# Optimization experiments

Hardware: AMD Instinct MI355X
Metric: run time of the kernel (lower is better)

The kernel has to match this reference:

```python
import jax, jax.numpy as jnp
import numpy as np

B, N, D, P = 32, 16, 64, 8  # batch, num_objs, in_feat_dim, patch size
PAIRS = N * (N - 1)


def _conv_relu(x, W, b):
    # Conv2d(kernel=3, stride=1, padding=1) + ReLU, NCHW/OIHW layout
    y = jax.lax.conv_general_dilated(
        x, W, window_strides=(1, 1), padding='SAME',
        dimension_numbers=('NCHW', 'OIHW', 'NCHW'))
    return jax.nn.relu(y + b[None, :, None, None])


def setup_inputs() -> dict:
    key = jax.random.key(0)
    ks = jax.random.split(key, 12)
    x = jax.random.normal(ks[0], (B, N, D, P, P), jnp.float32)
    # g_idx: cols 0,1 index into the repeated pair axis of size N*(N-1); col 2 is a 0/1 mask
    i0 = jax.random.randint(ks[1], (B, PAIRS, 1), 0, PAIRS)
    i1 = jax.random.randint(ks[2], (B, PAIRS, 1), 0, PAIRS)
    m = jax.random.randint(ks[3], (B, PAIRS, 1), 0, 2)
    g_idx = jnp.concatenate([i0, i1, m], axis=2)

    def w(k, o, i):
        return jax.random.normal(k, (o, i, 3, 3), jnp.float32) * (1.0 / np.sqrt(i * 9.0))

    return {
        'x': x, 'g_idx': g_idx,
        'W_rel': w(ks[4], D, 2 * D), 'b_rel': jnp.zeros((D,), jnp.float32),
        'W_self': w(ks[5], D, D), 'b_self': jnp.zeros((D,), jnp.float32),
        'W_aff': w(ks[6], D, D), 'b_aff': jnp.zeros((D,), jnp.float32),
        'W_agg': w(ks[7], D, 2 * D), 'b_agg': jnp.zeros((D,), jnp.float32),
    }


def reference(x, g_idx, W_rel, b_rel, W_self, b_self, W_aff, b_aff, W_agg, b_agg):
    b, n, d, p, _ = x.shape
    pairs = n * (n - 1)
    s = x
    # x1: [B, N*(N-1), D, P, P]
    x1 = jnp.tile(x, (1, n - 1, 1, 1, 1))

    def gather_pair(col):
        idx = g_idx[:, :, col][:, :, None, None, None]  # [B, pairs, 1, 1, 1]
        idx = jnp.broadcast_to(idx, (b, pairs, d, p, p))
        return jnp.take_along_axis(x1, idx, axis=1)

    y1 = gather_pair(0)
    y2 = gather_pair(1)
    mask = g_idx[:, :, 2][:, :, None, None, None].astype(x.dtype)
    r = jnp.concatenate([y1, y2], axis=2) * mask  # [B, pairs, 2D, P, P]
    r = _conv_relu(r.reshape(-1, 2 * d, p, p), W_rel, b_rel)
    r = r.reshape(b, n, n - 1, d, p, p).sum(axis=2)  # scatter-sum per object

    xs = _conv_relu(x.reshape(-1, d, p, p), W_self, b_self).reshape(b, n, d, p, p)
    pred = xs + r
    a = _conv_relu(pred.reshape(-1, d, p, p), W_aff, b_aff).reshape(b, n, d, p, p)
    a = jnp.concatenate([a, s], axis=2)  # [B, N, 2D, P, P]
    out = _conv_relu(a.reshape(-1, 2 * d, p, p), W_agg, b_agg).reshape(b, n, d, p, p)
    return out
```

## Files before the change

### kernel.cpp

```cpp
#include <hip/hip_runtime.h>


#define NIMG 512
#define IMGSZ 4096

using bf16x8 = __attribute__((ext_vector_type(8))) short;
using f32x4  = __attribute__((ext_vector_type(4))) float;
using u16x8  = __attribute__((ext_vector_type(8))) unsigned short;

__device__ inline unsigned short f2bf(float f) {
  union { float f; unsigned u; } v; v.f = f;
  unsigned r = v.u + 0x7fffu + ((v.u >> 16) & 1u);
  return (unsigned short)(r >> 16);
}

__device__ inline f32x4 bf4_to_f32(uint2 p) {
  union { unsigned u; float f; } c;
  f32x4 r;
  c.u = (p.x & 0xffffu) << 16;  r[0] = c.f;
  c.u = (p.x & 0xffff0000u);    r[1] = c.f;
  c.u = (p.y & 0xffffu) << 16;  r[2] = c.f;
  c.u = (p.y & 0xffff0000u);    r[3] = c.f;
  return r;
}

__global__ __launch_bounds__(256) void prep_w(
    const float* __restrict__ Wr, const float* __restrict__ Ws,
    const float* __restrict__ Wa, const float* __restrict__ Wg,
    unsigned short* __restrict__ Wt)
{
  int idx = blockIdx.x * 256 + threadIdx.x;
  if (idx >= 221184) return;
  float v;
  if (idx < 73728) {
    int c = idx / 36864, r = idx % 36864;
    int t = r >> 12, oc = (r >> 6) & 63, ic = r & 63;
    v = (c == 0 ? Ws : Wa)[oc * 576 + ic * 9 + t];
  } else {
    int r2 = idx - 73728;
    int half = r2 / 73728, rr = r2 % 73728;
    int t = rr >> 13, oc = (rr >> 7) & 63, ic = rr & 127;
    v = (half ? Wg : Wr)[oc * 1152 + ic * 9 + t];
  }
  Wt[idx] = f2bf(v);
}

__device__ inline void decode_img(int j, int& b, int& o) {
  b = ((j >> 7) << 3) | (j & 7);
  o = (j >> 3) & 15;
}

template<int ROWX>
__device__ inline void stage_x(const float* __restrict__ xb,
                               unsigned short* __restrict__ s,
                               int coff, int w, int px) {
#pragma unroll
  for (int r = 0; r < 8; ++r) {
    int ic0 = (w + 4 * r) * 2;
    const float* sp = xb + ic0 * 64;
    float a = sp[px], c = sp[64 + px];
    *(unsigned*)(s + px * ROWX + coff + ic0) =
        (unsigned)f2bf(a) | ((unsigned)f2bf(c) << 16);
  }
}

__global__ __launch_bounds__(256) void k1(
    const float* __restrict__ x,
    const unsigned short* __restrict__ Wt,
    unsigned short* __restrict__ cA, unsigned short* __restrict__ cB)
{
  constexpr int ROW = 72;
  __shared__ __align__(16) unsigned short sX[65 * ROW];
  int b, o;
  decode_img(blockIdx.x, b, o);
  const int img = b * 16 + o;
  const int tid = threadIdx.x;
  const int w = tid >> 6, lane = tid & 63;

  stage_x<ROW>(x + (size_t)img * IMGSZ, sX, 0, w, lane);
  if (tid < 36) ((unsigned*)(sX + 64 * ROW))[tid] = 0;
  __syncthreads();

  const int q = lane >> 4, n16 = lane & 15;
  const int ocb = w * 16;
  const int co = ocb + q * 4;

  int pyt[4], pxt[4];
#pragma unroll
  for (int t = 0; t < 4; ++t) { int p = t * 16 + n16; pyt[t] = p >> 3; pxt[t] = p & 7; }

  f32x4 aA[4] = {}, aB[4] = {};
  const unsigned short* WA = Wt + 73728 + (ocb + n16) * 128 + q * 8;
  const unsigned short* WB = WA + 64;
#pragma unroll
  for (int tap = 0; tap < 9; ++tap) {
    const int dy = tap / 3 - 1, dx = tap % 3 - 1;
    int spt[4];
#pragma unroll
    for (int t = 0; t < 4; ++t) {
      int sy = pyt[t] + dy, sx = pxt[t] + dx;
      spt[t] = ((unsigned)sy < 8u && (unsigned)sx < 8u) ? (sy * 8 + sx) : 64;
    }
#pragma unroll
    for (int ks = 0; ks < 2; ++ks) {
      bf16x8 aa = *(const bf16x8*)(WA + tap * 8192 + ks * 32);
      bf16x8 ab = *(const bf16x8*)(WB + tap * 8192 + ks * 32);
#pragma unroll
      for (int t = 0; t < 4; ++t) {
        bf16x8 bt = *(const bf16x8*)(sX + spt[t] * ROW + ks * 32 + q * 8);
        aA[t] = __builtin_amdgcn_mfma_f32_16x16x32_bf16(aa, bt, aA[t], 0, 0, 0);
        aB[t] = __builtin_amdgcn_mfma_f32_16x16x32_bf16(ab, bt, aB[t], 0, 0, 0);
      }
    }
  }

  const size_t ib = (size_t)img * IMGSZ;
#pragma unroll
  for (int t = 0; t < 4; ++t) {
    int p = t * 16 + n16;
    uint2 pa, pb;
    pa.x = (unsigned)f2bf(aA[t][0]) | ((unsigned)f2bf(aA[t][1]) << 16);
    pa.y = (unsigned)f2bf(aA[t][2]) | ((unsigned)f2bf(aA[t][3]) << 16);
    pb.x = (unsigned)f2bf(aB[t][0]) | ((unsigned)f2bf(aB[t][1]) << 16);
    pb.y = (unsigned)f2bf(aB[t][2]) | ((unsigned)f2bf(aB[t][3]) << 16);
    *(uint2*)(cA + ib + p * 64 + co) = pa;
    *(uint2*)(cB + ib + p * 64 + co) = pb;
  }
}

__global__ __launch_bounds__(256, 2) void k2(
    const float* __restrict__ x,
    const int* __restrict__ g_idx,
    const unsigned short* __restrict__ Wt,
    const float* __restrict__ b_rel, const float* __restrict__ b_self,
    const float* __restrict__ b_aff, const float* __restrict__ b_agg,
    const unsigned short* __restrict__ cA, const unsigned short* __restrict__ cB,
    float* __restrict__ out)
{
  constexpr int ROW = 72, ROW2 = 136, XROW = 68;
  __shared__ __align__(16) unsigned short sX[65 * ROW2];
  __shared__ __align__(16) unsigned short sPred[65 * ROW];
  __shared__ __align__(16) float sXS[64 * XROW];
  __shared__ int so1[15], so2[15];
  __shared__ float sm[15];

  int b, i;
  decode_img(blockIdx.x, b, i);
  const int img = b * 16 + i;
  const int tid = threadIdx.x;
  const int w = tid >> 6, lane = tid & 63;

  if (tid < 15) {
    const int* gp = g_idx + ((size_t)b * 240 + i * 15 + tid) * 3;
    so1[tid] = gp[0] & 15;
    so2[tid] = gp[1] & 15;
    sm[tid]  = (float)gp[2];
  }

  stage_x<ROW2>(x + (size_t)img * IMGSZ, sX, 64, w, lane);
  if (tid < 68) ((unsigned*)(sX + 64 * ROW2))[tid] = 0;
  if (tid < 36) ((unsigned*)(sPred + 64 * ROW))[tid] = 0;
  __syncthreads();

  const int q = lane >> 4, n16 = lane & 15;
  const int ocb = w * 16;
  const int co = ocb + q * 4;
  const int aw64  = (ocb + n16) * 64 + q * 8;
  const int aw128 = (ocb + n16) * 128 + q * 8;

  int pyt[4], pxt[4];
#pragma unroll
  for (int t = 0; t < 4; ++t) { int p = t * 16 + n16; pyt[t] = p >> 3; pxt[t] = p & 7; }

  {
    f32x4 f[4] = {};
    const unsigned short* WS = Wt + aw64;
#pragma unroll
    for (int tap = 0; tap < 9; ++tap) {
      const int dy = tap / 3 - 1, dx = tap % 3 - 1;
      int spt[4];
#pragma unroll
      for (int t = 0; t < 4; ++t) {
        int sy = pyt[t] + dy, sx = pxt[t] + dx;
        spt[t] = ((unsigned)sy < 8u && (unsigned)sx < 8u) ? (sy * 8 + sx) : 64;
      }
#pragma unroll
      for (int ks = 0; ks < 2; ++ks) {
        bf16x8 a = *(const bf16x8*)(WS + tap * 4096 + ks * 32);
#pragma unroll
        for (int t = 0; t < 4; ++t) {
          bf16x8 bt = *(const bf16x8*)(sX + spt[t] * ROW2 + 64 + ks * 32 + q * 8);
          f[t] = __builtin_amdgcn_mfma_f32_16x16x32_bf16(a, bt, f[t], 0, 0, 0);
        }
      }
    }
#pragma unroll
    for (int t = 0; t < 4; ++t) {
      int p = t * 16 + n16;
      f32x4 vs = f[t];
#pragma unroll
      for (int r = 0; r < 4; ++r) vs[r] = fmaxf(vs[r] + b_self[co + r], 0.f);
      *(f32x4*)(sXS + p * XROW + co) = vs;
    }
  }
  __syncthreads();

  {
    const size_t bb = (size_t)b * 16 * IMGSZ;
#pragma unroll 1
    for (int pass = 0; pass < 4; ++pass) {
      const int e = tid * 4 + pass * 1024;
      const int e_px = e >> 6, e_ic = e & 63;
      uint2 v1[15], v2[15];
#pragma unroll
      for (int j = 0; j < 15; ++j) {
        v1[j] = *(const uint2*)(cA + bb + (size_t)so1[j] * IMGSZ + e);
        v2[j] = *(const uint2*)(cB + bb + (size_t)so2[j] * IMGSZ + e);
      }
      f32x4 xv = *(const f32x4*)(sXS + e_px * XROW + e_ic);
      float acc[4], br[4];
#pragma unroll
      for (int r = 0; r < 4; ++r) { br[r] = b_rel[e_ic + r]; acc[r] = xv[r]; }
#pragma unroll
      for (int j = 0; j < 15; ++j) {
        float m = sm[j];
        f32x4 a1 = bf4_to_f32(v1[j]);
        f32x4 a2 = bf4_to_f32(v2[j]);
#pragma unroll
        for (int r = 0; r < 4; ++r)
          acc[r] += fmaxf(m * (a1[r] + a2[r]) + br[r], 0.f);
      }
      uint2 pk;
      pk.x = (unsigned)f2bf(acc[0]) | ((unsigned)f2bf(acc[1]) << 16);
      pk.y = (unsigned)f2bf(acc[2]) | ((unsigned)f2bf(acc[3]) << 16);
      *(uint2*)(sPred + e_px * ROW + e_ic) = pk;
    }
  }
  __syncthreads();

  {
    f32x4 f[4] = {};
    const unsigned short* WA = Wt + 36864 + aw64;
#pragma unroll
    for (int tap = 0; tap < 9; ++tap) {
      const int dy = tap / 3 - 1, dx = tap % 3 - 1;
      int spt[4];
#pragma unroll
      for (int t = 0; t < 4; ++t) {
        int sy = pyt[t] + dy, sx = pxt[t] + dx;
        spt[t] = ((unsigned)sy < 8u && (unsigned)sx < 8u) ? (sy * 8 + sx) : 64;
      }
#pragma unroll
      for (int ks = 0; ks < 2; ++ks) {
        bf16x8 a = *(const bf16x8*)(WA + tap * 4096 + ks * 32);
#pragma unroll
        for (int t = 0; t < 4; ++t) {
          bf16x8 bt = *(const bf16x8*)(sPred + spt[t] * ROW + ks * 32 + q * 8);
          f[t] = __builtin_amdgcn_mfma_f32_16x16x32_bf16(a, bt, f[t], 0, 0, 0);
        }
      }
    }
#pragma unroll
    for (int t = 0; t < 4; ++t) {
      int p = t * 16 + n16;
      float v0 = fmaxf(f[t][0] + b_aff[co + 0], 0.f);
      float v1 = fmaxf(f[t][1] + b_aff[co + 1], 0.f);
      float v2 = fmaxf(f[t][2] + b_aff[co + 2], 0.f);
      float v3 = fmaxf(f[t][3] + b_aff[co + 3], 0.f);
      uint2 pk;
      pk.x = (unsigned)f2bf(v0) | ((unsigned)f2bf(v1) << 16);
      pk.y = (unsigned)f2bf(v2) | ((unsigned)f2bf(v3) << 16);
      *(uint2*)(sX + p * ROW2 + co) = pk;
    }
  }
  __syncthreads();

  {
    f32x4 g[4] = {};
    const unsigned short* WG = Wt + 147456 + aw128;
#pragma unroll
    for (int tap = 0; tap < 9; ++tap) {
      const int dy = tap / 3 - 1, dx = tap % 3 - 1;
      int spt[4];
#pragma unroll
      for (int t = 0; t < 4; ++t) {
        int sy = pyt[t] + dy, sx = pxt[t] + dx;
        spt[t] = ((unsigned)sy < 8u && (unsigned)sx < 8u) ? (sy * 8 + sx) : 64;
      }
#pragma unroll
      for (int ks = 0; ks < 4; ++ks) {
        bf16x8 a = *(const bf16x8*)(WG + tap * 8192 + ks * 32);
#pragma unroll
        for (int t = 0; t < 4; ++t) {
          bf16x8 bt = *(const bf16x8*)(sX + spt[t] * ROW2 + ks * 32 + q * 8);
          g[t] = __builtin_amdgcn_mfma_f32_16x16x32_bf16(a, bt, g[t], 0, 0, 0);
        }
      }
    }
    float* ob = out + (size_t)img * IMGSZ;
#pragma unroll
    for (int t = 0; t < 4; ++t) {
      int p = t * 16 + n16;
#pragma unroll
      for (int r = 0; r < 4; ++r)
        ob[(co + r) * 64 + p] = fmaxf(g[t][r] + b_agg[co + r], 0.f);
    }
  }
}

extern "C" void kernel_launch(void* const* d_in, const int* in_sizes, int n_in,
                              void* d_out, int out_size, void* d_ws, size_t ws_size,
                              hipStream_t stream) {
  const float* x      = (const float*)d_in[0];
  const int*   g_idx  = (const int*)  d_in[1];
  const float* W_rel  = (const float*)d_in[2];
  const float* b_rel  = (const float*)d_in[3];
  const float* W_self = (const float*)d_in[4];
  const float* b_self = (const float*)d_in[5];
  const float* W_aff  = (const float*)d_in[6];
  const float* b_aff  = (const float*)d_in[7];
  const float* W_agg  = (const float*)d_in[8];
  const float* b_agg  = (const float*)d_in[9];
  float* out = (float*)d_out;

  unsigned short* cA = (unsigned short*)d_ws;
  unsigned short* cB = cA + 2097152;
  unsigned short* Wt = cB + 2097152;

  prep_w<<<864, 256, 0, stream>>>(W_rel, W_self, W_aff, W_agg, Wt);
  k1<<<NIMG, 256, 0, stream>>>(x, Wt, cA, cB);
  k2<<<NIMG, 256, 0, stream>>>(x, g_idx, Wt, b_rel, b_self, b_aff, b_agg,
                               cA, cB, out);
}
```

Measured before the change: 117.7 us.

## Fold weight prep into k1 and software-pipeline gathered relation loads in k2

Removes the separate weight-conversion launch. k1 now reads and converts W_rel directly from fp32 in its inner loop, and extra blocks convert the self/aff/agg weights in the same launch. In k2, the first pass of gathered cA/cB loads is issued before the self convolution, and each later pass's loads are prefetched while the current pass is reduced. This hides gather latency, at the cost of more registers and strided fp32 weight reads in k1.

```diff
diff --git a/kernel.cpp b/kernel.cpp
--- a/kernel.cpp
+++ b/kernel.cpp
@@ -24,27 +24,6 @@
   return r;
 }
 
-__global__ __launch_bounds__(256) void prep_w(
-    const float* __restrict__ Wr, const float* __restrict__ Ws,
-    const float* __restrict__ Wa, const float* __restrict__ Wg,
-    unsigned short* __restrict__ Wt)
-{
-  int idx = blockIdx.x * 256 + threadIdx.x;
-  if (idx >= 221184) return;
-  float v;
-  if (idx < 73728) {
-    int c = idx / 36864, r = idx % 36864;
-    int t = r >> 12, oc = (r >> 6) & 63, ic = r & 63;
-    v = (c == 0 ? Ws : Wa)[oc * 576 + ic * 9 + t];
-  } else {
-    int r2 = idx - 73728;
-    int half = r2 / 73728, rr = r2 % 73728;
-    int t = rr >> 13, oc = (rr >> 7) & 63, ic = rr & 127;
-    v = (half ? Wg : Wr)[oc * 1152 + ic * 9 + t];
-  }
-  Wt[idx] = f2bf(v);
-}
-
 __device__ inline void decode_img(int j, int& b, int& o) {
   b = ((j >> 7) << 3) | (j & 7);
   o = (j >> 3) & 15;
@@ -66,15 +45,38 @@
 
 __global__ __launch_bounds__(256) void k1(
     const float* __restrict__ x,
-    const unsigned short* __restrict__ Wt,
+    const float* __restrict__ Wr, const float* __restrict__ Ws,
+    const float* __restrict__ Wa, const float* __restrict__ Wg,
+    unsigned short* __restrict__ Wt,
     unsigned short* __restrict__ cA, unsigned short* __restrict__ cB)
 {
   constexpr int ROW = 72;
   __shared__ __align__(16) unsigned short sX[65 * ROW];
+  const int bid = blockIdx.x;
+  const int tid = threadIdx.x;
+
+  if (bid >= 512) {
+    int idx = (bid - 512) * 256 + tid;
+    float v;
+    unsigned short* dst;
+    if (idx < 73728) {
+      int c = idx / 36864, r = idx % 36864;
+      int t = r >> 12, oc = (r >> 6) & 63, ic = r & 63;
+      v = (c == 0 ? Ws : Wa)[oc * 576 + ic * 9 + t];
+      dst = Wt + idx;
+    } else {
+      int rr = idx - 73728;
+      int t = rr >> 13, oc = (rr >> 7) & 63, ic = rr & 127;
+      v = Wg[oc * 1152 + ic * 9 + t];
+      dst = Wt + 147456 + rr;
+    }
+    *dst = f2bf(v);
+    return;
+  }
+
   int b, o;
-  decode_img(blockIdx.x, b, o);
+  decode_img(bid, b, o);
   const int img = b * 16 + o;
-  const int tid = threadIdx.x;
   const int w = tid >> 6, lane = tid & 63;
 
   stage_x<ROW>(x + (size_t)img * IMGSZ, sX, 0, w, lane);
@@ -90,9 +92,8 @@
   for (int t = 0; t < 4; ++t) { int p = t * 16 + n16; pyt[t] = p >> 3; pxt[t] = p & 7; }
 
   f32x4 aA[4] = {}, aB[4] = {};
-  const unsigned short* WA = Wt + 73728 + (ocb + n16) * 128 + q * 8;
-  const unsigned short* WB = WA + 64;
-#pragma unroll
+  const float* WRbase = Wr + (ocb + n16) * 1152;
+#pragma unroll 1
   for (int tap = 0; tap < 9; ++tap) {
     const int dy = tap / 3 - 1, dx = tap % 3 - 1;
     int spt[4];
@@ -103,8 +104,13 @@
     }
 #pragma unroll
     for (int ks = 0; ks < 2; ++ks) {
-      bf16x8 aa = *(const bf16x8*)(WA + tap * 8192 + ks * 32);
-      bf16x8 ab = *(const bf16x8*)(WB + tap * 8192 + ks * 32);
+      const float* pA = WRbase + (ks * 32 + q * 8) * 9 + tap;
+      bf16x8 aa, ab;
+#pragma unroll
+      for (int e = 0; e < 8; ++e) {
+        aa[e] = (short)f2bf(pA[e * 9]);
+        ab[e] = (short)f2bf(pA[576 + e * 9]);
+      }
 #pragma unroll
       for (int t = 0; t < 4; ++t) {
         bf16x8 bt = *(const bf16x8*)(sX + spt[t] * ROW + ks * 32 + q * 8);
@@ -168,6 +174,17 @@
   const int aw64  = (ocb + n16) * 64 + q * 8;
   const int aw128 = (ocb + n16) * 128 + q * 8;
 
+  const size_t bb = (size_t)b * 16 * IMGSZ;
+  uint2 v1[15], v2[15];
+  {
+    const int e0 = tid * 4;
+#pragma unroll
+    for (int j = 0; j < 15; ++j) {
+      v1[j] = *(const uint2*)(cA + bb + (size_t)so1[j] * IMGSZ + e0);
+      v2[j] = *(const uint2*)(cB + bb + (size_t)so2[j] * IMGSZ + e0);
+    }
+  }
+
   int pyt[4], pxt[4];
 #pragma unroll
   for (int t = 0; t < 4; ++t) { int p = t * 16 + n16; pyt[t] = p >> 3; pxt[t] = p & 7; }
@@ -206,21 +223,27 @@
   __syncthreads();
 
   {
-    const size_t bb = (size_t)b * 16 * IMGSZ;
-#pragma unroll 1
+    const int e_ic = (tid * 4) & 63;
+    const int e_px0 = tid >> 4;
+    float br[4];
+#pragma unroll
+    for (int r = 0; r < 4; ++r) br[r] = b_rel[e_ic + r];
+#pragma unroll
     for (int pass = 0; pass < 4; ++pass) {
-      const int e = tid * 4 + pass * 1024;
-      const int e_px = e >> 6, e_ic = e & 63;
-      uint2 v1[15], v2[15];
-#pragma unroll
-      for (int j = 0; j < 15; ++j) {
-        v1[j] = *(const uint2*)(cA + bb + (size_t)so1[j] * IMGSZ + e);
-        v2[j] = *(const uint2*)(cB + bb + (size_t)so2[j] * IMGSZ + e);
-      }
+      uint2 n1[15], n2[15];
+      if (pass < 3) {
+        const int en = tid * 4 + (pass + 1) * 1024;
+#pragma unroll
+        for (int j = 0; j < 15; ++j) {
+          n1[j] = *(const uint2*)(cA + bb + (size_t)so1[j] * IMGSZ + en);
+          n2[j] = *(const uint2*)(cB + bb + (size_t)so2[j] * IMGSZ + en);
+        }
+      }
+      const int e_px = e_px0 + pass * 16;
       f32x4 xv = *(const f32x4*)(sXS + e_px * XROW + e_ic);
-      float acc[4], br[4];
-#pragma unroll
-      for (int r = 0; r < 4; ++r) { br[r] = b_rel[e_ic + r]; acc[r] = xv[r]; }
+      float acc[4];
+#pragma unroll
+      for (int r = 0; r < 4; ++r) acc[r] = xv[r];
 #pragma unroll
       for (int j = 0; j < 15; ++j) {
         float m = sm[j];
@@ -234,9 +257,17 @@
       pk.x = (unsigned)f2bf(acc[0]) | ((unsigned)f2bf(acc[1]) << 16);
       pk.y = (unsigned)f2bf(acc[2]) | ((unsigned)f2bf(acc[3]) << 16);
       *(uint2*)(sPred + e_px * ROW + e_ic) = pk;
-    }
-  }
-  __syncthreads();
+      if (pass < 3) {
+#pragma unroll
+        for (int j = 0; j < 15; ++j) { v1[j] = n1[j]; v2[j] = n2[j]; }
+      }
+    }
+  }
+  __syncthreads();
+
+  int pyt2[4], pxt2[4];
+#pragma unroll
+  for (int t = 0; t < 4; ++t) { int p = t * 16 + n16; pyt2[t] = p >> 3; pxt2[t] = p & 7; }
 
   {
     f32x4 f[4] = {};
@@ -247,7 +278,7 @@
       int spt[4];
 #pragma unroll
       for (int t = 0; t < 4; ++t) {
-        int sy = pyt[t] + dy, sx = pxt[t] + dx;
+        int sy = pyt2[t] + dy, sx = pxt2[t] + dx;
         spt[t] = ((unsigned)sy < 8u && (unsigned)sx < 8u) ? (sy * 8 + sx) : 64;
       }
 #pragma unroll
@@ -264,12 +295,12 @@
     for (int t = 0; t < 4; ++t) {
       int p = t * 16 + n16;
       float v0 = fmaxf(f[t][0] + b_aff[co + 0], 0.f);
-      float v1 = fmaxf(f[t][1] + b_aff[co + 1], 0.f);
-      float v2 = fmaxf(f[t][2] + b_aff[co + 2], 0.f);
+      float v1f = fmaxf(f[t][1] + b_aff[co + 1], 0.f);
+      float v2f = fmaxf(f[t][2] + b_aff[co + 2], 0.f);
       float v3 = fmaxf(f[t][3] + b_aff[co + 3], 0.f);
       uint2 pk;
-      pk.x = (unsigned)f2bf(v0) | ((unsigned)f2bf(v1) << 16);
-      pk.y = (unsigned)f2bf(v2) | ((unsigned)f2bf(v3) << 16);
+      pk.x = (unsigned)f2bf(v0) | ((unsigned)f2bf(v1f) << 16);
+      pk.y = (unsigned)f2bf(v2f) | ((unsigned)f2bf(v3) << 16);
       *(uint2*)(sX + p * ROW2 + co) = pk;
     }
   }
@@ -284,7 +315,7 @@
       int spt[4];
 #pragma unroll
       for (int t = 0; t < 4; ++t) {
-        int sy = pyt[t] + dy, sx = pxt[t] + dx;
+        int sy = pyt2[t] + dy, sx = pxt2[t] + dx;
         spt[t] = ((unsigned)sy < 8u && (unsigned)sx < 8u) ? (sy * 8 + sx) : 64;
       }
 #pragma unroll
@@ -327,8 +358,7 @@
   unsigned short* cB = cA + 2097152;
   unsigned short* Wt = cB + 2097152;
 
-  prep_w<<<864, 256, 0, stream>>>(W_rel, W_self, W_aff, W_agg, Wt);
-  k1<<<NIMG, 256, 0, stream>>>(x, Wt, cA, cB);
+  k1<<<512 + 576, 256, 0, stream>>>(x, W_rel, W_self, W_aff, W_agg, Wt, cA, cB);
   k2<<<NIMG, 256, 0, stream>>>(x, g_idx, Wt, b_rel, b_self, b_aff, b_agg,
                                cA, cB, out);
 }
```

Measured after the change: 184.3 us. 1.57x slower.

## Prefetch relation-gather loads ahead of self conv and double-buffer passes

Applied to the files above, without the earlier changes.

The first pass of pair-feature gathers from cA/cB is now issued before the self-convolution MFMA loop, so its global-memory latency overlaps that compute. The four gather passes are software-pipelined: each pass loads the next pass's 30 values into a second register set while accumulating the current one. The b_rel bias load is hoisted out of the pass loop, and two locals are renamed to avoid shadowing the new buffers. The cost is roughly 60 extra live registers, which could lower occupancy or cause spills.

```diff
diff --git a/kernel.cpp b/kernel.cpp
--- a/kernel.cpp
+++ b/kernel.cpp
@@ -168,6 +168,17 @@
   const int aw64  = (ocb + n16) * 64 + q * 8;
   const int aw128 = (ocb + n16) * 128 + q * 8;
 
+  const size_t bb = (size_t)b * 16 * IMGSZ;
+  uint2 v1[15], v2[15];
+  {
+    const int e0 = tid * 4;
+#pragma unroll
+    for (int j = 0; j < 15; ++j) {
+      v1[j] = *(const uint2*)(cA + bb + (size_t)so1[j] * IMGSZ + e0);
+      v2[j] = *(const uint2*)(cB + bb + (size_t)so2[j] * IMGSZ + e0);
+    }
+  }
+
   int pyt[4], pxt[4];
 #pragma unroll
   for (int t = 0; t < 4; ++t) { int p = t * 16 + n16; pyt[t] = p >> 3; pxt[t] = p & 7; }
@@ -206,21 +217,27 @@
   __syncthreads();
 
   {
-    const size_t bb = (size_t)b * 16 * IMGSZ;
-#pragma unroll 1
+    const int e_ic = (tid * 4) & 63;
+    const int e_px0 = tid >> 4;
+    float br[4];
+#pragma unroll
+    for (int r = 0; r < 4; ++r) br[r] = b_rel[e_ic + r];
+#pragma unroll
     for (int pass = 0; pass < 4; ++pass) {
-      const int e = tid * 4 + pass * 1024;
-      const int e_px = e >> 6, e_ic = e & 63;
-      uint2 v1[15], v2[15];
-#pragma unroll
-      for (int j = 0; j < 15; ++j) {
-        v1[j] = *(const uint2*)(cA + bb + (size_t)so1[j] * IMGSZ + e);
-        v2[j] = *(const uint2*)(cB + bb + (size_t)so2[j] * IMGSZ + e);
-      }
+      uint2 n1[15], n2[15];
+      if (pass < 3) {
+        const int en = tid * 4 + (pass + 1) * 1024;
+#pragma unroll
+        for (int j = 0; j < 15; ++j) {
+          n1[j] = *(const uint2*)(cA + bb + (size_t)so1[j] * IMGSZ + en);
+          n2[j] = *(const uint2*)(cB + bb + (size_t)so2[j] * IMGSZ + en);
+        }
+      }
+      const int e_px = e_px0 + pass * 16;
       f32x4 xv = *(const f32x4*)(sXS + e_px * XROW + e_ic);
-      float acc[4], br[4];
-#pragma unroll
-      for (int r = 0; r < 4; ++r) { br[r] = b_rel[e_ic + r]; acc[r] = xv[r]; }
+      float acc[4];
+#pragma unroll
+      for (int r = 0; r < 4; ++r) acc[r] = xv[r];
 #pragma unroll
       for (int j = 0; j < 15; ++j) {
         float m = sm[j];
@@ -234,6 +251,10 @@
       pk.x = (unsigned)f2bf(acc[0]) | ((unsigned)f2bf(acc[1]) << 16);
       pk.y = (unsigned)f2bf(acc[2]) | ((unsigned)f2bf(acc[3]) << 16);
       *(uint2*)(sPred + e_px * ROW + e_ic) = pk;
+      if (pass < 3) {
+#pragma unroll
+        for (int j = 0; j < 15; ++j) { v1[j] = n1[j]; v2[j] = n2[j]; }
+      }
     }
   }
   __syncthreads();
@@ -264,12 +285,12 @@
     for (int t = 0; t < 4; ++t) {
       int p = t * 16 + n16;
       float v0 = fmaxf(f[t][0] + b_aff[co + 0], 0.f);
-      float v1 = fmaxf(f[t][1] + b_aff[co + 1], 0.f);
-      float v2 = fmaxf(f[t][2] + b_aff[co + 2], 0.f);
+      float v1f = fmaxf(f[t][1] + b_aff[co + 1], 0.f);
+      float v2f = fmaxf(f[t][2] + b_aff[co + 2], 0.f);
       float v3 = fmaxf(f[t][3] + b_aff[co + 3], 0.f);
       uint2 pk;
-      pk.x = (unsigned)f2bf(v0) | ((unsigned)f2bf(v1) << 16);
-      pk.y = (unsigned)f2bf(v2) | ((unsigned)f2bf(v3) << 16);
+      pk.x = (unsigned)f2bf(v0) | ((unsigned)f2bf(v1f) << 16);
+      pk.y = (unsigned)f2bf(v2f) | ((unsigned)f2bf(v3) << 16);
       *(uint2*)(sX + p * ROW2 + co) = pk;
     }
   }
```

New measurement: 123.5 us. 1.05x slower.
